# Kernel tuning notes

Measured on AMD Instinct MI355X. Metric: run time of the kernel, lower is better.

The kernel has to match this reference:

```python
import jax, jax.numpy as jnp
import numpy as np

N, E = 50000, 800000
F_IN, H, P, C = 128, 64, 16, 40
L = 3  # gcn_layers


def setup_inputs() -> dict:
    key = jax.random.key(0)
    ks = jax.random.split(key, 10)
    s = 0.05
    return {
        "x_h": jax.random.normal(ks[0], (N, F_IN), jnp.float32),
        "pos_feat": jax.random.normal(ks[1], (N, P), jnp.float32),
        "edge_index": jax.random.randint(ks[2], (2, E), 0, N, dtype=jnp.int32),
        "W_pos": jax.random.normal(ks[3], (P, H), jnp.float32) * s,
        "b_pos": jnp.zeros((H,), jnp.float32),
        "W_init": jax.random.normal(ks[4], (F_IN, H), jnp.float32) * s,
        "b_init": jnp.zeros((H,), jnp.float32),
        "W_l": jax.random.normal(ks[5], (L, H, H), jnp.float32) * s,  # neighbor weight
        "W_r": jax.random.normal(ks[6], (L, H, H), jnp.float32) * s,  # root weight
        "b_conv": jnp.zeros((L, H), jnp.float32),
        "W_last": jax.random.normal(ks[7], (H, C), jnp.float32) * s,
        "b_last": jnp.zeros((C,), jnp.float32),
    }


def _sage_conv(x, src, dst, Wl, Wr, b):
    # PyG SAGEConv(aggr='mean'): out_i = Wl @ mean_{j in N(i)} x_j + Wr @ x_i + b
    msgs = x[src]  # [E, H] gather of source-node features
    agg = jax.ops.segment_sum(msgs, dst, num_segments=N)
    cnt = jax.ops.segment_sum(jnp.ones((E,), x.dtype), dst, num_segments=N)
    agg = agg / jnp.clip(cnt, 1.0, None)[:, None]  # mean; deg-0 nodes -> 0
    return agg @ Wl + x @ Wr + b


def reference(x_h, pos_feat, edge_index, W_pos, b_pos, W_init, b_init,
              W_l, W_r, b_conv, W_last, b_last):
    src, dst = edge_index[0], edge_index[1]
    # pos_embedding -> (hyperbolic encode simplified to identity in Euclidean manifold) -> tanh
    hyp_pos = jnp.tanh(pos_feat @ W_pos + b_pos)  # [N, H]
    h = x_h @ W_init + b_init  # [N, H]
    for i in range(L):
        h = _sage_conv(h, src, dst, W_l[i], W_r[i], b_conv[i])
        if i != L - 1:
            h = h + hyp_pos       # run_base == 'False' branch
            h = jax.nn.relu(h)    # dropout is no-op in eval mode
    emb = h @ W_last + b_last     # [N, C]
    return emb, jax.nn.log_softmax(emb, axis=1)
```

## Files before the change

### kernel.cpp

```cpp
#include <hip/hip_runtime.h>
#include <hip/hip_bf16.h>

#define NN 50000
#define NE 800000
#define FIN 128
#define HD 64
#define NC 40
#define RSPAN 6250
#define FBLK 3128
#define XG   782

typedef __hip_bfloat16 bf16;
typedef __attribute__((ext_vector_type(8))) short bf16x8;
typedef __attribute__((ext_vector_type(4))) float f32x4;

__device__ __forceinline__ void acc8(float* a, uint4 v){
  a[0] += __uint_as_float(v.x << 16); a[1] += __uint_as_float(v.x & 0xffff0000u);
  a[2] += __uint_as_float(v.y << 16); a[3] += __uint_as_float(v.y & 0xffff0000u);
  a[4] += __uint_as_float(v.z << 16); a[5] += __uint_as_float(v.z & 0xffff0000u);
  a[6] += __uint_as_float(v.w << 16); a[7] += __uint_as_float(v.w & 0xffff0000u);
}

__device__ __forceinline__ unsigned pack2(float lo, float hi){
  union { bf16 b; unsigned short u; } a, b;
  a.b = __float2bfloat16(lo);
  b.b = __float2bfloat16(hi);
  return (unsigned)a.u | ((unsigned)b.u << 16);
}

__device__ __forceinline__ short f2bf_bits(float f){
  union { bf16 b; short s; } u;
  u.b = __float2bfloat16(f);
  return u.s;
}

__device__ __forceinline__ void init_body(
    int wid, const float* __restrict__ x, const float* __restrict__ pos,
    const float* __restrict__ Wi, const float* __restrict__ bi,
    const float* __restrict__ Wp, const float* __restrict__ bp,
    bf16* __restrict__ h0b, bf16* __restrict__ hypb, int lane){
  const int quad = lane >> 4;
  const int col  = lane & 15;
  const int nw   = XG * 4;

  bf16x8 wif[4][4];
  #pragma unroll
  for (int ct = 0; ct < 4; ++ct)
    #pragma unroll
    for (int kf = 0; kf < 4; ++kf)
      #pragma unroll
      for (int j = 0; j < 8; ++j)
        wif[ct][kf][j] = f2bf_bits(Wi[(kf*32 + quad*8 + j)*HD + ct*16 + col]);
  bf16x8 wpf[4];
  #pragma unroll
  for (int ct = 0; ct < 4; ++ct)
    #pragma unroll
    for (int j = 0; j < 8; ++j){
      const int k = quad*8 + j;
      wpf[ct][j] = (k < 16) ? f2bf_bits(Wp[k*HD + ct*16 + col]) : (short)0;
    }
  float bih[4], bph[4];
  #pragma unroll
  for (int c = 0; c < 4; ++c){ bih[c] = bi[c*16 + col]; bph[c] = bp[c*16 + col]; }

  for (int t = wid; t < NN/16; t += nw){
    const int n0 = t * 16;
    bf16x8 af[4];
    #pragma unroll
    for (int kf = 0; kf < 4; ++kf){
      const float* xr = x + (size_t)(n0 + col)*FIN + kf*32 + quad*8;
      const float4 f0 = *(const float4*)xr;
      const float4 f1 = *(const float4*)(xr + 4);
      af[kf][0] = f2bf_bits(f0.x); af[kf][1] = f2bf_bits(f0.y);
      af[kf][2] = f2bf_bits(f0.z); af[kf][3] = f2bf_bits(f0.w);
      af[kf][4] = f2bf_bits(f1.x); af[kf][5] = f2bf_bits(f1.y);
      af[kf][6] = f2bf_bits(f1.z); af[kf][7] = f2bf_bits(f1.w);
    }
    bf16x8 ap;
    #pragma unroll
    for (int j = 0; j < 8; ++j) ap[j] = 0;
    if (quad < 2){
      const float* pr = pos + (size_t)(n0 + col)*16 + quad*8;
      const float4 p0 = *(const float4*)pr;
      const float4 p1 = *(const float4*)(pr + 4);
      ap[0] = f2bf_bits(p0.x); ap[1] = f2bf_bits(p0.y);
      ap[2] = f2bf_bits(p0.z); ap[3] = f2bf_bits(p0.w);
      ap[4] = f2bf_bits(p1.x); ap[5] = f2bf_bits(p1.y);
      ap[6] = f2bf_bits(p1.z); ap[7] = f2bf_bits(p1.w);
    }
    f32x4 ah[4], app[4];
    #pragma unroll
    for (int c = 0; c < 4; ++c){
      ah[c]  = (f32x4){bih[c], bih[c], bih[c], bih[c]};
      app[c] = (f32x4){bph[c], bph[c], bph[c], bph[c]};
    }
    #pragma unroll
    for (int ct = 0; ct < 4; ++ct){
      #pragma unroll
      for (int kf = 0; kf < 4; ++kf)
        ah[ct] = __builtin_amdgcn_mfma_f32_16x16x32_bf16(af[kf], wif[ct][kf], ah[ct], 0, 0, 0);
      app[ct] = __builtin_amdgcn_mfma_f32_16x16x32_bf16(ap, wpf[ct], app[ct], 0, 0, 0);
    }
    #pragma unroll
    for (int reg = 0; reg < 4; ++reg){
      const int n = n0 + quad*4 + reg;
      #pragma unroll
      for (int c = 0; c < 4; ++c){
        h0b[(size_t)n*HD + c*16 + col]  = __float2bfloat16(ah[c][reg]);
        hypb[(size_t)n*HD + c*16 + col] = __float2bfloat16(tanhf(app[c][reg]));
      }
    }
  }
}

__global__ __launch_bounds__(256) void k_fillinit(
    const int* __restrict__ ei, int* __restrict__ cursorp, int* __restrict__ esrc,
    const float* __restrict__ x, const float* __restrict__ pos,
    const float* __restrict__ Wi, const float* __restrict__ bi,
    const float* __restrict__ Wp, const float* __restrict__ bp,
    bf16* __restrict__ h0b, bf16* __restrict__ hypb){
  if (blockIdx.x < FBLK){
    const int chunk = blockIdx.x >> 3;
    const int lo    = (blockIdx.x & 7) * RSPAN;
    const int hi    = lo + RSPAN;
    int e = chunk * 2048 + threadIdx.x;
    #pragma unroll
    for (int j = 0; j < 8; ++j, e += 256){
      if (e < NE){
        const int d = ei[NE + e];
        if (d >= lo && d < hi){
          const int p = atomicAdd(&cursorp[d << 2], 1);
          if (p < 64) esrc[(d << 6) + p] = ei[e];
        }
      }
    }
    return;
  }
  init_body((blockIdx.x - FBLK) * 4 + (threadIdx.x >> 6),
            x, pos, Wi, bi, Wp, bp, h0b, hypb, threadIdx.x & 63);
}

__global__ __launch_bounds__(256) void k_xform(
    const bf16* __restrict__ h, const float* __restrict__ Wl,
    const float* __restrict__ Wr, const float* __restrict__ bc,
    const bf16* __restrict__ hypb, const int use_hyp,
    bf16* __restrict__ y, bf16* __restrict__ z){
  const int lane = threadIdx.x & 63;
  const int quad = lane >> 4;
  const int col  = lane & 15;
  const int wid  = blockIdx.x * 4 + (threadIdx.x >> 6);
  const int nw   = gridDim.x * 4;

  bf16x8 bfr[8][2];
  #pragma unroll
  for (int ct = 0; ct < 8; ++ct){
    const float* W = (ct < 4) ? Wl : Wr;
    const int nc = (ct & 3) * 16 + col;
    #pragma unroll
    for (int kf = 0; kf < 2; ++kf)
      #pragma unroll
      for (int j = 0; j < 8; ++j)
        bfr[ct][kf][j] = f2bf_bits(W[(kf*32 + quad*8 + j)*HD + nc]);
  }
  float zb[4];
  #pragma unroll
  for (int c = 0; c < 4; ++c) zb[c] = bc[c*16 + col];

  for (int t = wid; t < NN/16; t += nw){
    const int n0 = t * 16;
    union { uint4 u; bf16x8 v; } a0, a1;
    a0.u = *(const uint4*)(h + (size_t)(n0 + col)*HD + quad*8);
    a1.u = *(const uint4*)(h + (size_t)(n0 + col)*HD + 32 + quad*8);
    f32x4 acc[8];
    #pragma unroll
    for (int c = 0; c < 4; ++c) acc[c] = (f32x4){0.f, 0.f, 0.f, 0.f};
    #pragma unroll
    for (int c = 0; c < 4; ++c) acc[4+c] = (f32x4){zb[c], zb[c], zb[c], zb[c]};
    #pragma unroll
    for (int ct = 0; ct < 8; ++ct){
      acc[ct] = __builtin_amdgcn_mfma_f32_16x16x32_bf16(a0.v, bfr[ct][0], acc[ct], 0, 0, 0);
      acc[ct] = __builtin_amdgcn_mfma_f32_16x16x32_bf16(a1.v, bfr[ct][1], acc[ct], 0, 0, 0);
    }
    #pragma unroll
    for (int reg = 0; reg < 4; ++reg){
      const int n = n0 + quad*4 + reg;
      #pragma unroll
      for (int c = 0; c < 4; ++c){
        y[(size_t)n*HD + c*16 + col] = __float2bfloat16(acc[c][reg]);
        float zv = acc[4+c][reg];
        if (use_hyp) zv += __bfloat162float(hypb[(size_t)n*HD + c*16 + col]);
        z[(size_t)n*HD + c*16 + col] = __float2bfloat16(zv);
      }
    }
  }
}

__global__ __launch_bounds__(256) void k_gather(
    const bf16* __restrict__ y, const bf16* __restrict__ z,
    const int* __restrict__ cursorp, const int* __restrict__ esrc,
    bf16* __restrict__ out, const int do_relu){
  const int lane  = threadIdx.x & 63;
  const int n     = blockIdx.x * 4 + (threadIdx.x >> 6);
  if (n >= NN) return;
  const int fq    = lane & 7;
  const int eslot = lane >> 3;
  const int deg   = min(cursorp[n << 2], 64);
  const int r0    = n << 6;
  const int r1    = r0 + deg;
  float a0[8] = {0,0,0,0,0,0,0,0};
  float a1[8] = {0,0,0,0,0,0,0,0};
  int e = r0 + eslot;
  for (; e + 8 < r1; e += 16){
    const int s0 = esrc[e];
    const int s1 = esrc[e + 8];
    const uint4 v0 = ((const uint4*)(y + (size_t)s0*HD))[fq];
    const uint4 v1 = ((const uint4*)(y + (size_t)s1*HD))[fq];
    acc8(a0, v0);
    acc8(a1, v1);
  }
  if (e < r1){
    const int s = esrc[e];
    const uint4 v = ((const uint4*)(y + (size_t)s*HD))[fq];
    acc8(a0, v);
  }
  #pragma unroll
  for (int j = 0; j < 8; ++j){
    float s = a0[j] + a1[j];
    s += __shfl_xor(s, 8, 64);
    s += __shfl_xor(s, 16, 64);
    s += __shfl_xor(s, 32, 64);
    a0[j] = s;
  }
  if (eslot == 0){
    const float inv = deg > 0 ? 1.f / (float)deg : 0.f;
    const uint4 zv = ((const uint4*)(z + (size_t)n*HD))[fq];
    float zf[8];
    zf[0] = __uint_as_float(zv.x << 16); zf[1] = __uint_as_float(zv.x & 0xffff0000u);
    zf[2] = __uint_as_float(zv.y << 16); zf[3] = __uint_as_float(zv.y & 0xffff0000u);
    zf[4] = __uint_as_float(zv.z << 16); zf[5] = __uint_as_float(zv.z & 0xffff0000u);
    zf[6] = __uint_as_float(zv.w << 16); zf[7] = __uint_as_float(zv.w & 0xffff0000u);
    float o[8];
    #pragma unroll
    for (int j = 0; j < 8; ++j){
      o[j] = a0[j]*inv + zf[j];
      if (do_relu) o[j] = fmaxf(o[j], 0.f);
    }
    uint4 pv;
    pv.x = pack2(o[0], o[1]);
    pv.y = pack2(o[2], o[3]);
    pv.z = pack2(o[4], o[5]);
    pv.w = pack2(o[6], o[7]);
    ((uint4*)(out + (size_t)n*HD))[fq] = pv;
  }
}

__global__ __launch_bounds__(256) void k_final(
    const bf16* __restrict__ hin, const float* __restrict__ Wl,
    const float* __restrict__ bl, float* __restrict__ out){
  const int lane = threadIdx.x & 63;
  const int quad = lane >> 4;
  const int col  = lane & 15;
  const int wid  = blockIdx.x * 4 + (threadIdx.x >> 6);
  const int nw   = gridDim.x * 4;

  bf16x8 wf[3][2];
  float bb[3];
  #pragma unroll
  for (int ct = 0; ct < 3; ++ct){
    const int nc = ct*16 + col;
    const bool valid = nc < NC;
    bb[ct] = valid ? bl[nc] : -1e30f;
    #pragma unroll
    for (int kf = 0; kf < 2; ++kf)
      #pragma unroll
      for (int j = 0; j < 8; ++j)
        wf[ct][kf][j] = valid ? f2bf_bits(Wl[(kf*32 + quad*8 + j)*NC + nc]) : (short)0;
  }

  for (int t = wid; t < NN/16; t += nw){
    const int n0 = t * 16;
    union { uint4 u; bf16x8 v; } a0, a1;
    a0.u = *(const uint4*)(hin + (size_t)(n0 + col)*HD + quad*8);
    a1.u = *(const uint4*)(hin + (size_t)(n0 + col)*HD + 32 + quad*8);
    f32x4 acc[3];
    #pragma unroll
    for (int ct = 0; ct < 3; ++ct){
      acc[ct] = (f32x4){bb[ct], bb[ct], bb[ct], bb[ct]};
      acc[ct] = __builtin_amdgcn_mfma_f32_16x16x32_bf16(a0.v, wf[ct][0], acc[ct], 0, 0, 0);
      acc[ct] = __builtin_amdgcn_mfma_f32_16x16x32_bf16(a1.v, wf[ct][1], acc[ct], 0, 0, 0);
    }
    #pragma unroll
    for (int reg = 0; reg < 4; ++reg){
      const float e0 = acc[0][reg], e1 = acc[1][reg], e2 = acc[2][reg];
      float vmax = fmaxf(fmaxf(e0, e1), e2);
      vmax = fmaxf(vmax, __shfl_xor(vmax, 1, 64));
      vmax = fmaxf(vmax, __shfl_xor(vmax, 2, 64));
      vmax = fmaxf(vmax, __shfl_xor(vmax, 4, 64));
      vmax = fmaxf(vmax, __shfl_xor(vmax, 8, 64));
      float s = __expf(e0 - vmax) + __expf(e1 - vmax) + __expf(e2 - vmax);
      s += __shfl_xor(s, 1, 64);
      s += __shfl_xor(s, 2, 64);
      s += __shfl_xor(s, 4, 64);
      s += __shfl_xor(s, 8, 64);
      const float off = vmax + __logf(s);
      const int n = n0 + quad*4 + reg;
      #pragma unroll
      for (int ct = 0; ct < 3; ++ct){
        const int nc = ct*16 + col;
        if (nc < NC){
          const float e = acc[ct][reg];
          out[(size_t)n*NC + nc]                 = e;
          out[(size_t)NN*NC + (size_t)n*NC + nc] = e - off;
        }
      }
    }
  }
}

extern "C" void kernel_launch(void* const* d_in, const int* in_sizes, int n_in,
                              void* d_out, int out_size, void* d_ws, size_t ws_size,
                              hipStream_t stream){
  (void)in_sizes; (void)n_in; (void)out_size; (void)ws_size;
  const float* x_h    = (const float*)d_in[0];
  const float* pos    = (const float*)d_in[1];
  const int*   ei     = (const int*)  d_in[2];
  const float* W_pos  = (const float*)d_in[3];
  const float* b_pos  = (const float*)d_in[4];
  const float* W_init = (const float*)d_in[5];
  const float* b_init = (const float*)d_in[6];
  const float* W_l    = (const float*)d_in[7];
  const float* W_r    = (const float*)d_in[8];
  const float* b_conv = (const float*)d_in[9];
  const float* W_last = (const float*)d_in[10];
  const float* b_last = (const float*)d_in[11];
  float* out = (float*)d_out;

  char* p = (char*)d_ws;
  auto alloc = [&](size_t bytes)->char*{
    char* r = p; p += (bytes + 255) & ~(size_t)255; return r;
  };
  bf16* hb0    = (bf16*)alloc((size_t)NN*HD*2);
  bf16* hb1    = (bf16*)alloc((size_t)NN*HD*2);
  bf16* yb     = (bf16*)alloc((size_t)NN*HD*2);
  bf16* zbuf   = (bf16*)alloc((size_t)NN*HD*2);
  bf16* hypb   = (bf16*)alloc((size_t)NN*HD*2);
  int* cursorp = (int*)alloc((size_t)NN*4*4);
  int* esrc    = (int*)alloc((size_t)NN*64*4);

  hipMemsetAsync(cursorp, 0, (size_t)NN*4*4, stream);
  k_fillinit<<<FBLK + XG, 256, 0, stream>>>(ei, cursorp, esrc, x_h, pos,
                                            W_init, b_init, W_pos, b_pos,
                                            hb0, hypb);
  bf16* cur = hb0;
  bf16* nxt = hb1;
  for (int l = 0; l < 3; ++l){
    const int last = (l == 2);
    k_xform <<<XG, 256, 0, stream>>>(cur, W_l + l*HD*HD, W_r + l*HD*HD,
                                     b_conv + l*HD, hypb, !last, yb, zbuf);
    k_gather<<<(NN + 3)/4, 256, 0, stream>>>(yb, zbuf, cursorp, esrc, nxt, !last);
    bf16* t = cur; cur = nxt; nxt = t;
  }
  k_final <<<XG, 256, 0, stream>>>(cur, W_last, b_last, out);
}
```

Before: 285.2 us.

## Build ELL adjacency via bucketed counting sort instead of global atomics

```diff
diff --git a/kernel.cpp b/kernel.cpp
--- a/kernel.cpp
+++ b/kernel.cpp
@@ -6,9 +6,10 @@
 #define FIN 128
 #define HD 64
 #define NC 40
-#define RSPAN 6250
-#define FBLK 3128
 #define XG   782
+#define NB   391
+#define NBK  782
+#define BW   64
 
 typedef __hip_bfloat16 bf16;
 typedef __attribute__((ext_vector_type(8))) short bf16x8;
@@ -113,31 +114,105 @@
   }
 }
 
-__global__ __launch_bounds__(256) void k_fillinit(
-    const int* __restrict__ ei, int* __restrict__ cursorp, int* __restrict__ esrc,
+__global__ __launch_bounds__(256) void k_hist(
+    const int* __restrict__ ei, int* __restrict__ hist, int* __restrict__ totals,
     const float* __restrict__ x, const float* __restrict__ pos,
     const float* __restrict__ Wi, const float* __restrict__ bi,
     const float* __restrict__ Wp, const float* __restrict__ bp,
     bf16* __restrict__ h0b, bf16* __restrict__ hypb){
-  if (blockIdx.x < FBLK){
-    const int chunk = blockIdx.x >> 3;
-    const int lo    = (blockIdx.x & 7) * RSPAN;
-    const int hi    = lo + RSPAN;
-    int e = chunk * 2048 + threadIdx.x;
-    #pragma unroll
-    for (int j = 0; j < 8; ++j, e += 256){
-      if (e < NE){
-        const int d = ei[NE + e];
-        if (d >= lo && d < hi){
-          const int p = atomicAdd(&cursorp[d << 2], 1);
-          if (p < 64) esrc[(d << 6) + p] = ei[e];
-        }
-      }
+  __shared__ int lh[NBK];
+  if (blockIdx.x < NB){
+    for (int i = threadIdx.x; i < NBK; i += 256) lh[i] = 0;
+    __syncthreads();
+    int e = blockIdx.x * 2048 + threadIdx.x;
+    #pragma unroll
+    for (int j = 0; j < 8; ++j, e += 256)
+      if (e < NE) atomicAdd(&lh[ei[NE + e] >> 6], 1);
+    __syncthreads();
+    for (int i = threadIdx.x; i < NBK; i += 256){
+      const int c = lh[i];
+      hist[i*NB + blockIdx.x] = c;
+      if (c) atomicAdd(&totals[i], c);
     }
     return;
   }
-  init_body((blockIdx.x - FBLK) * 4 + (threadIdx.x >> 6),
+  init_body((blockIdx.x - NB) * 4 + (threadIdx.x >> 6),
             x, pos, Wi, bi, Wp, bp, h0b, hypb, threadIdx.x & 63);
+}
+
+__global__ __launch_bounds__(512) void k_scan(
+    const int* __restrict__ hist, const int* __restrict__ totals,
+    int* __restrict__ ofs, int* __restrict__ baseA){
+  __shared__ int sc[512];
+  __shared__ int baseSh;
+  const int b = blockIdx.x;
+  const int t = threadIdx.x;
+  int part = 0;
+  for (int j = t; j < b; j += 512) part += totals[j];
+  sc[t] = part; __syncthreads();
+  for (int off = 256; off > 0; off >>= 1){
+    if (t < off) sc[t] += sc[t + off];
+    __syncthreads();
+  }
+  if (t == 0) baseSh = sc[0];
+  __syncthreads();
+  const int base = baseSh;
+  __syncthreads();
+  const int v = (t < NB) ? hist[b*NB + t] : 0;
+  sc[t] = v; __syncthreads();
+  for (int off = 1; off < 512; off <<= 1){
+    const int xv = (t >= off) ? sc[t - off] : 0;
+    __syncthreads();
+    sc[t] += xv;
+    __syncthreads();
+  }
+  if (t < NB) ofs[b*NB + t] = base + sc[t] - v;
+  if (t == 0) baseA[b] = base;
+  if (b == NBK - 1 && t == 0) baseA[NBK] = base + sc[511];
+}
+
+__global__ __launch_bounds__(256) void k_scatter(
+    const int* __restrict__ ei, const int* __restrict__ ofs,
+    int* __restrict__ packed){
+  __shared__ int cur[NBK];
+  for (int i = threadIdx.x; i < NBK; i += 256) cur[i] = ofs[i*NB + blockIdx.x];
+  __syncthreads();
+  int e = blockIdx.x * 2048 + threadIdx.x;
+  #pragma unroll
+  for (int j = 0; j < 8; ++j, e += 256){
+    if (e < NE){
+      const int d = ei[NE + e];
+      const int s = ei[e];
+      const int p = atomicAdd(&cur[d >> 6], 1);
+      packed[p] = s | ((d & 63) << 16);
+    }
+  }
+}
+
+__global__ __launch_bounds__(256) void k_ell(
+    const int* __restrict__ packed, const int* __restrict__ baseA,
+    int* __restrict__ esrc, int* __restrict__ degp){
+  __shared__ int cnt[BW];
+  __shared__ int ell[BW * 64];
+  if (threadIdx.x < BW) cnt[threadIdx.x] = 0;
+  __syncthreads();
+  const int b  = blockIdx.x;
+  const int lo = baseA[b], hi = baseA[b + 1];
+  for (int e = lo + threadIdx.x; e < hi; e += 256){
+    const int pk = packed[e];
+    const int dl = (pk >> 16) & 63;
+    const int p  = atomicAdd(&cnt[dl], 1);
+    if (p < 64) ell[dl*64 + p] = pk & 0xffff;
+  }
+  __syncthreads();
+  const int n0 = b * BW;
+  for (int i = threadIdx.x; i < BW * 16; i += 256){
+    const int node = i >> 4;
+    if (n0 + node < NN)
+      ((uint4*)(esrc + (size_t)(n0 + node)*64))[i & 15] = ((const uint4*)ell)[i];
+  }
+  for (int i = threadIdx.x; i < BW; i += 256)
+    if (n0 + i < NN) degp[n0 + i] = cnt[i];
 }
 
 __global__ __launch_bounds__(256) void k_xform(
@@ -197,14 +272,14 @@
 
 __global__ __launch_bounds__(256) void k_gather(
     const bf16* __restrict__ y, const bf16* __restrict__ z,
-    const int* __restrict__ cursorp, const int* __restrict__ esrc,
+    const int* __restrict__ degp, const int* __restrict__ esrc,
     bf16* __restrict__ out, const int do_relu){
   const int lane  = threadIdx.x & 63;
   const int n     = blockIdx.x * 4 + (threadIdx.x >> 6);
   if (n >= NN) return;
   const int fq    = lane & 7;
   const int eslot = lane >> 3;
-  const int deg   = min(cursorp[n << 2], 64);
+  const int deg   = min(degp[n], 64);
   const int r0    = n << 6;
   const int r1    = r0 + deg;
   float a0[8] = {0,0,0,0,0,0,0,0};
@@ -339,25 +414,34 @@
   auto alloc = [&](size_t bytes)->char*{
     char* r = p; p += (bytes + 255) & ~(size_t)255; return r;
   };
-  bf16* hb0    = (bf16*)alloc((size_t)NN*HD*2);
-  bf16* hb1    = (bf16*)alloc((size_t)NN*HD*2);
-  bf16* yb     = (bf16*)alloc((size_t)NN*HD*2);
-  bf16* zbuf   = (bf16*)alloc((size_t)NN*HD*2);
-  bf16* hypb   = (bf16*)alloc((size_t)NN*HD*2);
-  int* cursorp = (int*)alloc((size_t)NN*4*4);
-  int* esrc    = (int*)alloc((size_t)NN*64*4);
-
-  hipMemsetAsync(cursorp, 0, (size_t)NN*4*4, stream);
-  k_fillinit<<<FBLK + XG, 256, 0, stream>>>(ei, cursorp, esrc, x_h, pos,
-                                            W_init, b_init, W_pos, b_pos,
-                                            hb0, hypb);
+  bf16* hb0  = (bf16*)alloc((size_t)NN*HD*2);
+  bf16* hb1  = (bf16*)alloc((size_t)NN*HD*2);
+  bf16* yb   = (bf16*)alloc((size_t)NN*HD*2);
+  bf16* zbuf = (bf16*)alloc((size_t)NN*HD*2);
+  bf16* hypb = (bf16*)alloc((size_t)NN*HD*2);
+  int* esrc  = (int*)alloc((size_t)NN*64*4);
+  int* degp  = (int*)alloc((size_t)NN*4);
+
+  int* hist   = (int*)yb;
+  int* ofs    = hist + NBK*NB;
+  int* totals = ofs + NBK*NB;
+  int* baseA  = totals + NBK;
+  int* packed = (int*)zbuf;
+
+  hipMemsetAsync(totals, 0, (size_t)NBK*4, stream);
+  k_hist   <<<NB + XG, 256, 0, stream>>>(ei, hist, totals, x_h, pos,
+                                         W_init, b_init, W_pos, b_pos, hb0, hypb);
+  k_scan   <<<NBK, 512, 0, stream>>>(hist, totals, ofs, baseA);
+  k_scatter<<<NB, 256, 0, stream>>>(ei, ofs, packed);
+  k_ell    <<<NBK, 256, 0, stream>>>(packed, baseA, esrc, degp);
+
   bf16* cur = hb0;
   bf16* nxt = hb1;
   for (int l = 0; l < 3; ++l){
     const int last = (l == 2);
     k_xform <<<XG, 256, 0, stream>>>(cur, W_l + l*HD*HD, W_r + l*HD*HD,
                                      b_conv + l*HD, hypb, !last, yb, zbuf);
-    k_gather<<<(NN + 3)/4, 256, 0, stream>>>(yb, zbuf, cursorp, esrc, nxt, !last);
+    k_gather<<<(NN + 3)/4, 256, 0, stream>>>(yb, zbuf, degp, esrc, nxt, !last);
     bf16* t = cur; cur = nxt; nxt = t;
   }
   k_final <<<XG, 256, 0, stream>>>(cur, W_last, b_last, out);
```

After: 275.8 us. 3.3% less time.
